# Performance work log

Measured on AMD Instinct MI355X. Metric: run time of the kernel, lower is better.

## Reference

```python
import jax, jax.numpy as jnp
import numpy as np

N = 150000   # active voxels
C = 64       # channels
K = 27       # 3x3x3 kernel offsets


def sparse_conv(feat, nbr_idx, W):
    # feat: [N, C]; nbr_idx: [N, K] input-voxel index per kernel offset; W: [K, C, C]
    gathered = feat[nbr_idx]                       # [N, K, C] gather
    return jnp.einsum('nkc,kcd->nd', gathered, W)  # per-offset matmul + scatter-sum


def setup_inputs() -> dict:
    key = jax.random.key(0)
    k1, k2, k3, k4 = jax.random.split(key, 4)
    x = jax.random.normal(k1, (N, C), dtype=jnp.float32)
    nbr_idx = jax.random.randint(k2, (N, K), 0, N, dtype=jnp.int64)
    scale = 1.0 / np.sqrt(K * C)
    W0 = jax.random.normal(k3, (K, C, C), dtype=jnp.float32) * scale
    W1 = jax.random.normal(k4, (K, C, C), dtype=jnp.float32) * scale
    return {"x": x, "nbr_idx": nbr_idx, "W0": W0, "W1": W1}


def reference(x, nbr_idx, W0, W1):
    out = jax.nn.relu(sparse_conv(x, nbr_idx, W0))
    out = sparse_conv(out, nbr_idx, W1)
    out = jax.nn.relu(out + x)
    return out
```

## Files before the change

kernel.cpp:

```cpp
#include <hip/hip_runtime.h>
#include <stdint.h>


typedef __attribute__((ext_vector_type(8))) short short8;
typedef __attribute__((ext_vector_type(4))) float f32x4;

#define NV 150000
#define KOFF 27

static __device__ __forceinline__ ushort f2bf(float f) {
  union { float f; uint32_t u; } v; v.f = f;
  uint32_t u = v.u;
  return (ushort)((u + 0x7fffu + ((u >> 16) & 1u)) >> 16);
}

__global__ void prep_kernel(const float* __restrict__ x,
                            const float* __restrict__ W0,
                            const float* __restrict__ W1,
                            ushort* __restrict__ xb,
                            ushort* __restrict__ wp0,
                            ushort* __restrict__ wp1,
                            int nc4, int wtot) {
  int i = blockIdx.x * 256 + threadIdx.x;
  if (i < nc4) {
    float4 v = ((const float4*)x)[i];
    ushort4 o;
    o.x = f2bf(v.x); o.y = f2bf(v.y); o.z = f2bf(v.z); o.w = f2bf(v.w);
    ((ushort4*)xb)[i] = o;
    return;
  }
  int o = i - nc4;
  const float* W = W0;
  ushort* wp = wp0;
  if (o >= wtot) { o -= wtot; W = W1; wp = wp1; }
  if (o >= wtot) return;
  int j  = o & 7;
  int l  = (o >> 3) & 63;
  int ct = (o >> 9) & 3;
  int s  = (o >> 11) & 1;
  int k  = o >> 12;
  int c  = s * 32 + (l >> 4) * 8 + j;
  int d  = ct * 16 + (l & 15);
  wp[o] = f2bf(W[(k * 64 + c) * 64 + d]);
}

template <int MODE>
__global__ __launch_bounds__(256, 5) void conv_kernel(
    const ushort* __restrict__ feat,
    const int*    __restrict__ nbr,
    const ushort* __restrict__ wp,
    const float*  __restrict__ resid,
    ushort*       __restrict__ out_bf,
    float*        __restrict__ out_f,
    int n) {
  __shared__ __align__(16) int    sIdx[128 * KOFF];
  __shared__ __align__(16) ushort smB[2][4096];

  const int tid  = threadIdx.x;
  const int lane = tid & 63;
  const int wid  = tid >> 6;
  const int quad = lane >> 4;
  const int lo   = lane & 15;
  const int mw   = blockIdx.x * 128 + wid * 32;

  {
    const int total = n * KOFF;
    const int g0    = blockIdx.x * (128 * KOFF);
    #pragma unroll
    for (int u = 0; u < 3; ++u) {
      int j  = tid + 256 * u;
      int ai = g0 + 4 * j;
      ai = ai + 4 <= total ? ai : (total - 4);
      ((int4*)sIdx)[j] = *(const int4*)(nbr + ai);
    }
    if (tid < 96) {
      int j  = 768 + tid;
      int ai = g0 + 4 * j;
      ai = ai + 4 <= total ? ai : (total - 4);
      ((int4*)sIdx)[j] = *(const int4*)(nbr + ai);
    }
  }

  {
    #pragma unroll
    for (int u = 0; u < 2; ++u) {
      int c = wid * 2 + u;
      __builtin_amdgcn_global_load_lds(
          (const __attribute__((address_space(1))) void*)(wp + c * 512 + lane * 8),
          (__attribute__((address_space(3))) void*)(&smB[0][c * 512]), 16, 0, 0);
    }
  }
  __syncthreads();

  int ioff[2];
  #pragma unroll
  for (int rt = 0; rt < 2; ++rt) ioff[rt] = (wid * 32 + rt * 16 + lo) * KOFF;

  f32x4 acc[2][4];
  #pragma unroll
  for (int rt = 0; rt < 2; ++rt)
    #pragma unroll
    for (int ct = 0; ct < 4; ++ct)
      acc[rt][ct] = (f32x4)0.0f;

  int gi[2];
  #pragma unroll
  for (int rt = 0; rt < 2; ++rt) {
    int g = sIdx[ioff[rt]];
    gi[rt] = g < n ? g : 0;
  }

  #pragma unroll 1
  for (int k = 0; k < KOFF; ++k) {
    const int buf = k & 1;
    short8 a[2][2];
    #pragma unroll
    for (int rt = 0; rt < 2; ++rt) {
      const ushort* rowp = feat + gi[rt] * 64 + quad * 8;
      a[rt][0] = *(const short8*)(rowp);
      a[rt][1] = *(const short8*)(rowp + 32);
    }
    __builtin_amdgcn_sched_barrier(0);
    if (k + 1 < KOFF) {
      #pragma unroll
      for (int u = 0; u < 2; ++u) {
        int c = wid * 2 + u;
        __builtin_amdgcn_global_load_lds(
            (const __attribute__((address_space(1))) void*)(wp + (k + 1) * 4096 + c * 512 + lane * 8),
            (__attribute__((address_space(3))) void*)(&smB[buf ^ 1][c * 512]), 16, 0, 0);
      }
      #pragma unroll
      for (int rt = 0; rt < 2; ++rt) gi[rt] = sIdx[ioff[rt] + k + 1];
    }
    const short8* bl = (const short8*)smB[buf];
    short8 b[8];
    #pragma unroll
    for (int t = 0; t < 8; ++t) b[t] = bl[t * 64 + lane];
    #pragma unroll
    for (int s = 0; s < 2; ++s)
      #pragma unroll
      for (int rt = 0; rt < 2; ++rt)
        #pragma unroll
        for (int ct = 0; ct < 4; ++ct)
          acc[rt][ct] = __builtin_amdgcn_mfma_f32_16x16x32_bf16(a[rt][s], b[s * 4 + ct], acc[rt][ct], 0, 0, 0);
    __syncthreads();
  }

  #pragma unroll
  for (int rt = 0; rt < 2; ++rt) {
    int rbase = mw + rt * 16 + quad * 4;
    #pragma unroll
    for (int ct = 0; ct < 4; ++ct) {
      int col = ct * 16 + lo;
      #pragma unroll
      for (int j = 0; j < 4; ++j) {
        int r = rbase + j;
        if (r < n) {
          float v = acc[rt][ct][j];
          if (MODE == 0) {
            v = v > 0.0f ? v : 0.0f;
            out_bf[r * 64 + col] = f2bf(v);
          } else {
            v += resid[r * 64 + col];
            v = v > 0.0f ? v : 0.0f;
            out_f[r * 64 + col] = v;
          }
        }
      }
    }
  }
}

extern "C" void kernel_launch(void* const* d_in, const int* in_sizes, int n_in,
                              void* d_out, int out_size, void* d_ws, size_t ws_size,
                              hipStream_t stream) {
  const float* x   = (const float*)d_in[0];
  const int*   nbr = (const int*)d_in[1];
  const float* W0  = (const float*)d_in[2];
  const float* W1  = (const float*)d_in[3];
  float* out = (float*)d_out;

  const int n    = NV;
  const int nc   = NV * 64;
  const int nc4  = nc / 4;
  const int wtot = KOFF * 4096;

  ushort* xb  = (ushort*)d_ws;
  ushort* yb  = xb + nc;
  ushort* wp0 = yb + nc;
  ushort* wp1 = wp0 + wtot;

  const int prep_units = nc4 + 2 * wtot;
  prep_kernel<<<(prep_units + 255) / 256, 256, 0, stream>>>(x, W0, W1, xb, wp0, wp1, nc4, wtot);

  const int grid = (n + 127) / 128;
  conv_kernel<0><<<grid, 256, 0, stream>>>(xb, nbr, wp0, nullptr, yb, nullptr, n);
  conv_kernel<1><<<grid, 256, 0, stream>>>(yb, nbr, wp1, x, nullptr, out, n);
}
```

Before: 268.2 us.

## Prefetch next offset's gathered rows into double-buffered registers with manual waitcnts

Restructures the 27-offset loop so that the neighbour feature gather for offset k+1 is issued before the MFMAs of offset k. Two register sets alternate via a manually unrolled lambda, and the neighbour index is read two steps ahead. The end-of-iteration __syncthreads is replaced by explicit vmcnt waits plus a single s_barrier, and the first weight-tile LDS load is moved ahead of the index staging. The aim is to hide the latency of the random-row gather. In exchange, register pressure rises and the launch bound drops from 5 to 4 blocks per CU, reducing occupancy.

```diff
diff --git a/kernel.cpp b/kernel.cpp
--- a/kernel.cpp
+++ b/kernel.cpp
@@ -45,7 +45,7 @@
 }
 
 template <int MODE>
-__global__ __launch_bounds__(256, 5) void conv_kernel(
+__global__ __launch_bounds__(256, 4) void conv_kernel(
     const ushort* __restrict__ feat,
     const int*    __restrict__ nbr,
     const ushort* __restrict__ wp,
@@ -63,6 +63,14 @@
   const int lo   = lane & 15;
   const int mw   = blockIdx.x * 128 + wid * 32;
 
+  #pragma unroll
+  for (int u = 0; u < 2; ++u) {
+    int c = wid * 2 + u;
+    __builtin_amdgcn_global_load_lds(
+        (const __attribute__((address_space(1))) void*)(wp + c * 512 + lane * 8),
+        (__attribute__((address_space(3))) void*)(&smB[0][c * 512]), 16, 0, 0);
+  }
+
   {
     const int total = n * KOFF;
     const int g0    = blockIdx.x * (128 * KOFF);
@@ -81,16 +89,9 @@
     }
   }
 
-  {
-    #pragma unroll
-    for (int u = 0; u < 2; ++u) {
-      int c = wid * 2 + u;
-      __builtin_amdgcn_global_load_lds(
-          (const __attribute__((address_space(1))) void*)(wp + c * 512 + lane * 8),
-          (__attribute__((address_space(3))) void*)(&smB[0][c * 512]), 16, 0, 0);
-    }
-  }
-  __syncthreads();
+  asm volatile("s_waitcnt vmcnt(0) lgkmcnt(0)" ::: "memory");
+  __builtin_amdgcn_s_barrier();
+  __builtin_amdgcn_sched_barrier(0);
 
   int ioff[2];
   #pragma unroll
@@ -103,23 +104,52 @@
     for (int ct = 0; ct < 4; ++ct)
       acc[rt][ct] = (f32x4)0.0f;
 
-  int gi[2];
-  #pragma unroll
-  for (int rt = 0; rt < 2; ++rt) {
-    int g = sIdx[ioff[rt]];
-    gi[rt] = g < n ? g : 0;
-  }
-
-  #pragma unroll 1
-  for (int k = 0; k < KOFF; ++k) {
-    const int buf = k & 1;
-    short8 a[2][2];
+  short8 aA[2][2], aB[2][2];
+  int gA[2], gB[2];
+  {
+    int g0r[2];
     #pragma unroll
     for (int rt = 0; rt < 2; ++rt) {
-      const ushort* rowp = feat + gi[rt] * 64 + quad * 8;
-      a[rt][0] = *(const short8*)(rowp);
-      a[rt][1] = *(const short8*)(rowp + 32);
-    }
+      int g = sIdx[ioff[rt]];
+      g0r[rt] = g < n ? g : 0;
+    }
+    #pragma unroll
+    for (int rt = 0; rt < 2; ++rt) {
+      const ushort* rowp = feat + g0r[rt] * 64 + quad * 8;
+      aA[rt][0] = *(const short8*)(rowp);
+      aA[rt][1] = *(const short8*)(rowp + 32);
+    }
+    #pragma unroll
+    for (int rt = 0; rt < 2; ++rt) gA[rt] = sIdx[ioff[rt] + 1];
+  }
+
+  const short8* wv = (const short8*)wp;
+  (void)wv;
+
+  auto iter = [&](int k, short8 (&aC)[2][2], short8 (&aN)[2][2],
+                  int (&giN)[2], int (&gi2)[2]) {
+    if (k + 1 < KOFF) {
+      #pragma unroll
+      for (int rt = 0; rt < 2; ++rt) {
+        int g = giN[rt];
+        g = g < n ? g : 0;
+        const ushort* rowp = feat + g * 64 + quad * 8;
+        aN[rt][0] = *(const short8*)(rowp);
+        aN[rt][1] = *(const short8*)(rowp + 32);
+      }
+    }
+    if (k + 2 < KOFF) {
+      #pragma unroll
+      for (int rt = 0; rt < 2; ++rt) gi2[rt] = sIdx[ioff[rt] + k + 2];
+    }
+    __builtin_amdgcn_sched_barrier(0);
+    if (k + 1 < KOFF) {
+      asm volatile("s_waitcnt vmcnt(4)" ::: "memory");
+    } else {
+      asm volatile("s_waitcnt vmcnt(0)" ::: "memory");
+    }
+    __builtin_amdgcn_sched_barrier(0);
+    __builtin_amdgcn_s_barrier();
     __builtin_amdgcn_sched_barrier(0);
     if (k + 1 < KOFF) {
       #pragma unroll
@@ -127,12 +157,10 @@
         int c = wid * 2 + u;
         __builtin_amdgcn_global_load_lds(
             (const __attribute__((address_space(1))) void*)(wp + (k + 1) * 4096 + c * 512 + lane * 8),
-            (__attribute__((address_space(3))) void*)(&smB[buf ^ 1][c * 512]), 16, 0, 0);
+            (__attribute__((address_space(3))) void*)(&smB[(k + 1) & 1][c * 512]), 16, 0, 0);
       }
-      #pragma unroll
-      for (int rt = 0; rt < 2; ++rt) gi[rt] = sIdx[ioff[rt] + k + 1];
-    }
-    const short8* bl = (const short8*)smB[buf];
+    }
+    const short8* bl = (const short8*)smB[k & 1];
     short8 b[8];
     #pragma unroll
     for (int t = 0; t < 8; ++t) b[t] = bl[t * 64 + lane];
@@ -142,9 +170,15 @@
       for (int rt = 0; rt < 2; ++rt)
         #pragma unroll
         for (int ct = 0; ct < 4; ++ct)
-          acc[rt][ct] = __builtin_amdgcn_mfma_f32_16x16x32_bf16(a[rt][s], b[s * 4 + ct], acc[rt][ct], 0, 0, 0);
-    __syncthreads();
-  }
+          acc[rt][ct] = __builtin_amdgcn_mfma_f32_16x16x32_bf16(aC[rt][s], b[s * 4 + ct], acc[rt][ct], 0, 0, 0);
+  };
+
+  #pragma unroll 1
+  for (int k = 0; k < KOFF - 1; k += 2) {
+    iter(k,     aA, aB, gA, gB);
+    iter(k + 1, aB, aA, gB, gA);
+  }
+  iter(KOFF - 1, aA, aB, gA, gB);
 
   #pragma unroll
   for (int rt = 0; rt < 2; ++rt) {
```

Result: slower. 290.0 us (+8.1%).

## Split bf16 features into channel-half planes and reorder K loop by half

Applied to the files above, without the earlier changes.

Features are stored as two planes of 32 channels each, so each gather pulls a 64-byte half-row rather than a full 128-byte row. The K loop now iterates over 54 (offset, half) pairs, two per step, with weights repacked to match that order. Each pass then touches only one half-plane (about 9.6 MB), which may fit better in cache and improve locality of the random gathers. The cost is more, smaller gather transactions and a little extra index arithmetic. The first weight tile's LDS load is also issued before the index load to overlap the two.

```diff
diff --git a/kernel.cpp b/kernel.cpp
--- a/kernel.cpp
+++ b/kernel.cpp
@@ -26,7 +26,12 @@
     float4 v = ((const float4*)x)[i];
     ushort4 o;
     o.x = f2bf(v.x); o.y = f2bf(v.y); o.z = f2bf(v.z); o.w = f2bf(v.w);
-    ((ushort4*)xb)[i] = o;
+    int f    = i << 2;
+    int nrow = f >> 6;
+    int c    = f & 63;
+    int h    = c >> 5;
+    int off  = nrow * 32 + (c & 31);
+    ((ushort4*)(xb + (size_t)h * NV * 32))[off >> 2] = o;
     return;
   }
   int o = i - nc4;
@@ -34,13 +39,14 @@
   ushort* wp = wp0;
   if (o >= wtot) { o -= wtot; W = W1; wp = wp1; }
   if (o >= wtot) return;
-  int j  = o & 7;
+  int jj = o & 7;
   int l  = (o >> 3) & 63;
   int ct = (o >> 9) & 3;
-  int s  = (o >> 11) & 1;
-  int k  = o >> 12;
-  int c  = s * 32 + (l >> 4) * 8 + j;
-  int d  = ct * 16 + (l & 15);
+  int t  = o >> 11;
+  int h  = t >= KOFF ? 1 : 0;
+  int k  = t - h * KOFF;
+  int c  = h * 32 + ((l >> 4) << 3) + jj;
+  int d  = (ct << 4) + (l & 15);
   wp[o] = f2bf(W[(k * 64 + c) * 64 + d]);
 }
 
@@ -63,6 +69,14 @@
   const int lo   = lane & 15;
   const int mw   = blockIdx.x * 128 + wid * 32;
 
+  #pragma unroll
+  for (int u = 0; u < 2; ++u) {
+    int c = wid * 2 + u;
+    __builtin_amdgcn_global_load_lds(
+        (const __attribute__((address_space(1))) void*)(wp + c * 512 + lane * 8),
+        (__attribute__((address_space(3))) void*)(&smB[0][c * 512]), 16, 0, 0);
+  }
+
   {
     const int total = n * KOFF;
     const int g0    = blockIdx.x * (128 * KOFF);
@@ -80,16 +94,6 @@
       ((int4*)sIdx)[j] = *(const int4*)(nbr + ai);
     }
   }
-
-  {
-    #pragma unroll
-    for (int u = 0; u < 2; ++u) {
-      int c = wid * 2 + u;
-      __builtin_amdgcn_global_load_lds(
-          (const __attribute__((address_space(1))) void*)(wp + c * 512 + lane * 8),
-          (__attribute__((address_space(3))) void*)(&smB[0][c * 512]), 16, 0, 0);
-    }
-  }
   __syncthreads();
 
   int ioff[2];
@@ -103,46 +107,62 @@
     for (int ct = 0; ct < 4; ++ct)
       acc[rt][ct] = (f32x4)0.0f;
 
-  int gi[2];
+  int gi[2][2];
   #pragma unroll
   for (int rt = 0; rt < 2; ++rt) {
-    int g = sIdx[ioff[rt]];
-    gi[rt] = g < n ? g : 0;
+    gi[0][rt] = sIdx[ioff[rt] + 0];
+    gi[1][rt] = sIdx[ioff[rt] + 1];
   }
 
   #pragma unroll 1
-  for (int k = 0; k < KOFF; ++k) {
-    const int buf = k & 1;
+  for (int p = 0; p < KOFF; ++p) {
+    const int buf = p & 1;
+    const int j0 = 2 * p, j1 = 2 * p + 1;
+    const int h0 = j0 >= KOFF ? 1 : 0;
+    const int h1 = j1 >= KOFF ? 1 : 0;
+
     short8 a[2][2];
-    #pragma unroll
-    for (int rt = 0; rt < 2; ++rt) {
-      const ushort* rowp = feat + gi[rt] * 64 + quad * 8;
-      a[rt][0] = *(const short8*)(rowp);
-      a[rt][1] = *(const short8*)(rowp + 32);
+    {
+      const ushort* pl0 = feat + (size_t)h0 * n * 32;
+      const ushort* pl1 = feat + (size_t)h1 * n * 32;
+      #pragma unroll
+      for (int rt = 0; rt < 2; ++rt) {
+        int g0r = gi[0][rt]; g0r = g0r < n ? g0r : 0;
+        int g1r = gi[1][rt]; g1r = g1r < n ? g1r : 0;
+        a[0][rt] = *(const short8*)(pl0 + g0r * 32 + quad * 8);
+        a[1][rt] = *(const short8*)(pl1 + g1r * 32 + quad * 8);
+      }
     }
     __builtin_amdgcn_sched_barrier(0);
-    if (k + 1 < KOFF) {
+    if (p + 1 < KOFF) {
       #pragma unroll
       for (int u = 0; u < 2; ++u) {
         int c = wid * 2 + u;
         __builtin_amdgcn_global_load_lds(
-            (const __attribute__((address_space(1))) void*)(wp + (k + 1) * 4096 + c * 512 + lane * 8),
+            (const __attribute__((address_space(1))) void*)(wp + (p + 1) * 4096 + c * 512 + lane * 8),
             (__attribute__((address_space(3))) void*)(&smB[buf ^ 1][c * 512]), 16, 0, 0);
       }
-      #pragma unroll
-      for (int rt = 0; rt < 2; ++rt) gi[rt] = sIdx[ioff[rt] + k + 1];
-    }
-    const short8* bl = (const short8*)smB[buf];
-    short8 b[8];
-    #pragma unroll
-    for (int t = 0; t < 8; ++t) b[t] = bl[t * 64 + lane];
-    #pragma unroll
-    for (int s = 0; s < 2; ++s)
+      const int jn0 = 2 * (p + 1), jn1 = 2 * (p + 1) + 1;
+      const int kk0 = jn0 - (jn0 >= KOFF ? KOFF : 0);
+      const int kk1 = jn1 - (jn1 >= KOFF ? KOFF : 0);
+      #pragma unroll
+      for (int rt = 0; rt < 2; ++rt) {
+        gi[0][rt] = sIdx[ioff[rt] + kk0];
+        gi[1][rt] = sIdx[ioff[rt] + kk1];
+      }
+    }
+    #pragma unroll
+    for (int sub = 0; sub < 2; ++sub) {
+      const short8* bl = (const short8*)&smB[buf][sub * 2048];
+      short8 b[4];
+      #pragma unroll
+      for (int ct = 0; ct < 4; ++ct) b[ct] = bl[ct * 64 + lane];
       #pragma unroll
       for (int rt = 0; rt < 2; ++rt)
         #pragma unroll
         for (int ct = 0; ct < 4; ++ct)
-          acc[rt][ct] = __builtin_amdgcn_mfma_f32_16x16x32_bf16(a[rt][s], b[s * 4 + ct], acc[rt][ct], 0, 0, 0);
+          acc[rt][ct] = __builtin_amdgcn_mfma_f32_16x16x32_bf16(a[sub][rt], b[ct], acc[rt][ct], 0, 0, 0);
+    }
     __syncthreads();
   }
 
@@ -159,7 +179,7 @@
           float v = acc[rt][ct][j];
           if (MODE == 0) {
             v = v > 0.0f ? v : 0.0f;
-            out_bf[r * 64 + col] = f2bf(v);
+            out_bf[(size_t)(col >> 5) * n * 32 + r * 32 + (col & 31)] = f2bf(v);
           } else {
             v += resid[r * 64 + col];
             v = v > 0.0f ? v : 0.0f;
```

After: 331.9 us. +23.7%, slower.
